# Optimization experiments

Hardware: AMD Instinct MI355X
Metric: run time of the kernel (lower is better)

Reference implementation:

```python
import jax, jax.numpy as jnp
import numpy as np

D_IN, D_OUT, K = 128, 256, 16
B, N = 2, 16384
D_HALF = D_OUT // 2
EPS = 1e-6
GROUPS = 16


def conv1x1(x, w, b):
    # x: (B,C,N,K), w: (O,C), b: (O,)
    return jnp.einsum('oc,bcnk->bonk', w, x) + b[None, :, None, None]


def groupnorm(x, w, b, groups=GROUPS):
    Bv, C, Nv, Kv = x.shape
    xr = x.reshape(Bv, groups, C // groups, Nv, Kv)
    m = xr.mean(axis=(2, 3, 4), keepdims=True)
    v = xr.var(axis=(2, 3, 4), keepdims=True)
    xn = ((xr - m) / jnp.sqrt(v + EPS)).reshape(Bv, C, Nv, Kv)
    return xn * w[None, :, None, None] + b[None, :, None, None]


def lse(coords, x, idx, dist, w, b, gw, gb):
    # coords: (B,N,3); x: (B,C,N,1); idx: (B,N,K); dist: (B,N,K)
    nbr = jax.vmap(lambda c, i: c[i])(coords, idx)          # (B,N,K,3)
    ctr = jnp.broadcast_to(coords[:, :, None, :], nbr.shape)  # (B,N,K,3)
    rel = jnp.concatenate([ctr, nbr, ctr - nbr], axis=-1)    # (B,N,K,9)
    geo = jnp.concatenate([rel.transpose(0, 3, 1, 2), dist[:, None, :, :]], axis=1)  # (B,10,N,K)
    geo = jax.nn.relu(groupnorm(conv1x1(geo, w, b), gw, gb))  # (B,d/2,N,K)
    nf = jax.vmap(lambda f, i: f[:, i])(x[..., 0], idx)       # (B,d/2,N,K)
    return jnp.concatenate([geo, nf], axis=1)                 # (B,d,N,K)


def attentive_pool(x, w, b, gw, gb):
    m = x.mean(axis=-1, keepdims=True)  # (B,C,N,1)
    return jax.nn.relu(groupnorm(conv1x1(m, w, b), gw, gb))


def setup_inputs() -> dict:
    key = jax.random.key(0)
    ks = jax.random.split(key, 16)
    s = 0.02
    d = {
        'coords': jax.random.normal(ks[0], (B, N, 3), jnp.float32),
        'features': jax.random.normal(ks[1], (B, D_IN, N, 1), jnp.float32),
        'knn_dist': jax.random.uniform(ks[2], (B, N, K), jnp.float32),
        'knn_idx': jax.random.randint(ks[3], (B, N, K), 0, N),
        'w1': jax.random.normal(ks[4], (D_HALF, D_IN), jnp.float32) * s,
        'b1': jnp.zeros((D_HALF,), jnp.float32),
        'lse1_w': jax.random.normal(ks[5], (D_HALF, 10), jnp.float32) * s,
        'lse1_b': jnp.zeros((D_HALF,), jnp.float32),
        'lse1_gw': jnp.ones((D_HALF,), jnp.float32),
        'lse1_gb': jnp.zeros((D_HALF,), jnp.float32),
        'pool1_w': jax.random.normal(ks[6], (D_HALF, D_OUT), jnp.float32) * s,
        'pool1_b': jnp.zeros((D_HALF,), jnp.float32),
        'pool1_gw': jnp.ones((D_HALF,), jnp.float32),
        'pool1_gb': jnp.zeros((D_HALF,), jnp.float32),
        'lse2_w': jax.random.normal(ks[7], (D_HALF, 10), jnp.float32) * s,
        'lse2_b': jnp.zeros((D_HALF,), jnp.float32),
        'lse2_gw': jnp.ones((D_HALF,), jnp.float32),
        'lse2_gb': jnp.zeros((D_HALF,), jnp.float32),
        'pool2_w': jax.random.normal(ks[8], (D_OUT, D_OUT), jnp.float32) * s,
        'pool2_b': jnp.zeros((D_OUT,), jnp.float32),
        'pool2_gw': jnp.ones((D_OUT,), jnp.float32),
        'pool2_gb': jnp.zeros((D_OUT,), jnp.float32),
        'mlp2_w': jax.random.normal(ks[9], (2 * D_OUT, D_OUT), jnp.float32) * s,
        'mlp2_b': jnp.zeros((2 * D_OUT,), jnp.float32),
        'sc_w': jax.random.normal(ks[10], (2 * D_OUT, D_IN), jnp.float32) * s,
        'sc_b': jnp.zeros((2 * D_OUT,), jnp.float32),
        'sc_gw': jnp.ones((2 * D_OUT,), jnp.float32),
        'sc_gb': jnp.zeros((2 * D_OUT,), jnp.float32),
    }
    return d


def reference(coords, features, knn_dist, knn_idx,
              w1, b1,
              lse1_w, lse1_b, lse1_gw, lse1_gb,
              pool1_w, pool1_b, pool1_gw, pool1_gb,
              lse2_w, lse2_b, lse2_gw, lse2_gb,
              pool2_w, pool2_b, pool2_gw, pool2_gb,
              mlp2_w, mlp2_b, sc_w, sc_b, sc_gw, sc_gb):
    # mlp1: conv + LeakyReLU(0.2), no norm
    x = jax.nn.leaky_relu(conv1x1(features, w1, b1), 0.2)        # (B,d/2,N,1)
    x = lse(coords, x, knn_idx, knn_dist, lse1_w, lse1_b, lse1_gw, lse1_gb)  # (B,d,N,K)
    x = attentive_pool(x, pool1_w, pool1_b, pool1_gw, pool1_gb)  # (B,d/2,N,1)
    x = lse(coords, x, knn_idx, knn_dist, lse2_w, lse2_b, lse2_gw, lse2_gb)  # (B,d,N,K)
    x = attentive_pool(x, pool2_w, pool2_b, pool2_gw, pool2_gb)  # (B,d,N,1)
    main = conv1x1(x, mlp2_w, mlp2_b)                            # (B,2d,N,1)
    short = groupnorm(conv1x1(features, sc_w, sc_b), sc_gw, sc_gb)
    return jax.nn.leaky_relu(main + short, 0.01)                 # (B,2d,N,1)
```

## Files before the change

### kernel.cpp

```cpp
#include <hip/hip_runtime.h>


constexpr int Bc = 2;
constexpr int Nc = 16384;
constexpr int Kc = 16;
constexpr float EPSc = 1e-6f;

typedef __attribute__((ext_vector_type(8))) short short8;
typedef __attribute__((ext_vector_type(4))) short short4v;
typedef __attribute__((ext_vector_type(4))) float floatx4;

__device__ inline short f2bf(float x) {
    union { float f; unsigned u; } v; v.f = x;
    unsigned r = v.u + 0x7fffu + ((v.u >> 16) & 1u);
    return (short)(r >> 16);
}
__device__ inline float bf2f(short s) {
    union { unsigned u; float f; } v;
    v.u = ((unsigned)(unsigned short)s) << 16;
    return v.f;
}

constexpr size_t OW_P1W = 0;
constexpr size_t OW_P2W = OW_P1W + 128*256;
constexpr size_t OW_M2W = OW_P2W + 256*256;
constexpr size_t OW_SCW = OW_M2W + 512*256;
constexpr size_t OW_W1  = OW_SCW + 512*128;
constexpr size_t OW_L1W = OW_W1  + 128*128;
constexpr size_t OW_L2W = OW_L1W + 128*32;
constexpr size_t OW_FB  = OW_L2W + 128*32;
constexpr size_t OW_X1  = OW_FB  + (size_t)Bc*Nc*128;
constexpr size_t OW_M   = OW_X1  + (size_t)Bc*Nc*128;
constexpr size_t OW_Z1  = OW_M   + (size_t)Bc*Nc*256;
constexpr size_t OW_Z2  = OW_Z1  + (size_t)Bc*Nc*128;
constexpr size_t OW_S   = OW_Z2  + (size_t)Bc*Nc*256;

constexpr int CV0 = 128*256;
constexpr int CV1 = CV0 + 256*256;
constexpr int CV2 = CV1 + 512*256;
constexpr int CV3 = CV2 + 512*128;
constexpr int CV4 = CV3 + 128*128;
constexpr int CV5 = CV4 + 128*32;
constexpr int CV6 = CV5 + 128*32;
constexpr int CVTOT = CV6 + 512;
constexpr int PREP_BLKS = (CVTOT + 255) / 256;
constexpr int FEAT_BLKS = Bc * Nc / 64;

__launch_bounds__(256)
__global__ void prep_feat_kernel(const float* __restrict__ p1w,
                                 const float* __restrict__ p2w,
                                 const float* __restrict__ m2w,
                                 const float* __restrict__ scw,
                                 const float* __restrict__ w1,
                                 const float* __restrict__ l1w,
                                 const float* __restrict__ l2w,
                                 short* __restrict__ W16,
                                 float* __restrict__ ST,
                                 const float* __restrict__ fin,
                                 short* __restrict__ fout)
{
    const int blk = blockIdx.x;
    const int tid = threadIdx.x;
    if (blk < PREP_BLKS) {
        int i = blk * 256 + tid;
        if (i < CV0) { W16[OW_P1W + i] = f2bf(p1w[i]); return; }
        if (i < CV1) { int k = i - CV0; W16[OW_P2W + k] = f2bf(p2w[k]); return; }
        if (i < CV2) { int k = i - CV1; W16[OW_M2W + k] = f2bf(m2w[k]); return; }
        if (i < CV3) { int k = i - CV2; W16[OW_SCW + k] = f2bf(scw[k]); return; }
        if (i < CV4) { int k = i - CV3; W16[OW_W1  + k] = f2bf(w1[k]); return; }
        if (i < CV5) { int k = i - CV4; int o = k >> 5, c = k & 31;
                       W16[OW_L1W + k] = (c < 10) ? f2bf(l1w[o*10+c]) : (short)0; return; }
        if (i < CV6) { int k = i - CV5; int o = k >> 5, c = k & 31;
                       W16[OW_L2W + k] = (c < 10) ? f2bf(l2w[o*10+c]) : (short)0; return; }
        { int k = i - CV6; if (k < 512) ST[k] = 0.f; }
        return;
    }
    const int fb  = blk - PREP_BLKS;
    int lane = tid & 63, wave = tid >> 6;
    int bb = fb / (Nc / 64);
    int n  = (fb % (Nc / 64)) * 64 + lane;
    #pragma unroll
    for (int cc = 0; cc < 4; cc++) {
        int c0 = (wave + cc * 4) * 8;
        short8 sv;
        #pragma unroll
        for (int i = 0; i < 8; i++)
            sv[i] = f2bf(fin[((size_t)bb * 128 + c0 + i) * Nc + n]);
        *(short8*)&fout[((size_t)(bb * Nc + n)) * 128 + c0] = sv;
    }
}

__launch_bounds__(256)
__global__ void geo_reduce_kernel(const float* __restrict__ coords,
                                  const int* __restrict__ knn_idx,
                                  const float* __restrict__ knn_dist,
                                  float* __restrict__ dst)
{
    __shared__ float part[4][65];
    const int tid  = threadIdx.x;
    const int b    = blockIdx.y;
    const int base = blockIdx.x * 256 + tid;
    const float* cb  = coords   + (size_t)b * Nc * 3;
    const int*   ib  = knn_idx  + (size_t)b * Nc * Kc;
    const float* db  = knn_dist + (size_t)b * Nc * Kc;

    float acc[65];
    #pragma unroll
    for (int i = 0; i < 65; i++) acc[i] = 0.f;

    #pragma unroll
    for (int it = 0; it < 4; it++) {
        int r = base + it * 65536;
        int n = r >> 4;
        float cx = cb[n*3+0], cy = cb[n*3+1], cz = cb[n*3+2];
        int   j  = ib[r];
        float nx = cb[j*3+0], ny = cb[j*3+1], nz = cb[j*3+2];
        float d  = db[r];
        float g[10] = {cx,cy,cz,nx,ny,nz,cx-nx,cy-ny,cz-nz,d};
        #pragma unroll
        for (int c = 0; c < 10; c++) acc[c] += g[c];
        int idx = 10;
        #pragma unroll
        for (int c = 0; c < 10; c++)
            #pragma unroll
            for (int c2 = c; c2 < 10; c2++) acc[idx++] += g[c] * g[c2];
    }
    #pragma unroll
    for (int i = 0; i < 65; i++) {
        float v = acc[i];
        #pragma unroll
        for (int off = 1; off < 64; off <<= 1) v += __shfl_xor(v, off);
        acc[i] = v;
    }
    int lane = tid & 63, wave = tid >> 6;
    if (lane == 0) {
        #pragma unroll
        for (int i = 0; i < 65; i++) part[wave][i] = acc[i];
    }
    __syncthreads();
    if (tid < 65) {
        float s = part[0][tid] + part[1][tid] + part[2][tid] + part[3][tid];
        atomicAdd(&dst[b * 65 + tid], s);
    }
}

__launch_bounds__(512)
__global__ void lse_param_kernel(const float* __restrict__ geoS,
                                 const float* __restrict__ l1w,
                                 const float* __restrict__ l1b,
                                 const float* __restrict__ l1gw,
                                 const float* __restrict__ l1gb,
                                 const float* __restrict__ l2w,
                                 const float* __restrict__ l2b,
                                 const float* __restrict__ l2gw,
                                 const float* __restrict__ l2gb,
                                 float* __restrict__ lp)
{
    __shared__ float osum[512], osq[512];
    const int tid = threadIdx.x;
    const int s = tid >> 8, r = tid & 255, b = r >> 7, o = r & 127;
    const float* wf = s ? l2w : l1w;
    const float* bf = s ? l2b : l1b;
    const float* gwf = s ? l2gw : l1gw;
    const float* gbf = s ? l2gb : l1gb;
    const float NK = (float)(Nc * Kc);
    const float* S = geoS + b * 65;

    float w[10];
    #pragma unroll
    for (int c = 0; c < 10; c++) w[c] = wf[o * 10 + c];
    float wS = 0.f;
    #pragma unroll
    for (int c = 0; c < 10; c++) wS += w[c] * S[c];
    float q = 0.f;
    {
        int idx = 10;
        #pragma unroll
        for (int c = 0; c < 10; c++)
            #pragma unroll
            for (int c2 = c; c2 < 10; c2++) {
                float t = w[c] * w[c2] * S[idx++];
                q += (c == c2) ? t : 2.f * t;
            }
    }
    float bo = bf[o];
    osum[tid] = NK * bo + wS;
    osq[tid]  = NK * bo * bo + 2.f * bo * wS + q;
    __syncthreads();
    int gb0 = tid & ~7;
    float gs = 0.f, gq = 0.f;
    #pragma unroll
    for (int i = 0; i < 8; i++) { gs += osum[gb0 + i]; gq += osq[gb0 + i]; }
    float cnt  = 8.f * NK;
    float mean = gs / cnt;
    float var  = gq / cnt - mean * mean;
    float iv   = rsqrtf(var + EPSc);
    float psc  = iv * gwf[o];
    float psh  = (bo - mean) * psc + gbf[o];
    lp[s * 512 + b * 256 + o]       = psc;
    lp[s * 512 + b * 256 + 128 + o] = psh;
}

template<int CIN, int COUT, int GROUP_CH, int MODE>
__launch_bounds__(256)
__global__ void gemm_conv(const short* __restrict__ wA,
                          const short* __restrict__ xB,
                          const float* __restrict__ bias,
                          short* __restrict__ outb,
                          float* __restrict__ outf,
                          float* __restrict__ stats,
                          const short* __restrict__ sbuf,
                          const float* __restrict__ st_sc,
                          const float* __restrict__ gw,
                          const float* __restrict__ gb,
                          float sc_cnt,
                          const float* __restrict__ bst,
                          const float* __restrict__ bgw,
                          const float* __restrict__ bgb,
                          float bcnt,
                          const float* __restrict__ bias2,
                          short* __restrict__ outb2)
{
    __shared__ short Abuf[128 * 68];
    __shared__ short Bbuf[128 * 68];
    __shared__ float sstat[32];
    __shared__ float smean[4], sinv[4];
    __shared__ float bsc[256], bsh[256];

    const int tid  = threadIdx.x;
    const int n0   = blockIdx.x * 128;
    const int mo   = blockIdx.y * 128;
    const int b    = blockIdx.z;
    const int lane = tid & 63;
    const int wave = tid >> 6;
    const int wm   = (wave >> 1) * 64;
    const int wn   = (wave & 1) * 64;
    const int l15  = lane & 15;
    const int quad = lane >> 4;
    const bool sc_tile = (MODE == 4) && (mo < 512);

    if constexpr (MODE == 2 || MODE == 4) { if (tid < 32) sstat[tid] = 0.f; }
    if constexpr (MODE == 3) {
        if (tid < 4) {
            int g = (mo >> 5) + tid;
            float s0 = st_sc[(b * 16 + g) * 2 + 0];
            float s1 = st_sc[(b * 16 + g) * 2 + 1];
            float mean = s0 / sc_cnt;
            float var  = s1 / sc_cnt - mean * mean;
            smean[tid] = mean;
            sinv[tid]  = rsqrtf(var + EPSc);
        }
        if (tid < CIN) {
            int g = tid >> 4;
            float s0 = bst[(b * 16 + g) * 2 + 0];
            float s1 = bst[(b * 16 + g) * 2 + 1];
            float mean = s0 / bcnt;
            float var  = s1 / bcnt - mean * mean;
            float inv  = rsqrtf(var + EPSc);
            float sc_  = inv * bgw[tid];
            bsc[tid] = sc_;
            bsh[tid] = bgb[tid] - mean * sc_;
        }
    }

    floatx4 acc[4][4];
    #pragma unroll
    for (int mi = 0; mi < 4; mi++)
        #pragma unroll
        for (int ni = 0; ni < 4; ni++)
            acc[mi][ni] = (floatx4){0.f, 0.f, 0.f, 0.f};

    const short* wAr = wA + (size_t)mo * CIN;
    const short* xBr = xB + (size_t)b * Nc * CIN + (size_t)n0 * CIN;

    for (int c0 = 0; c0 < CIN; c0 += 64) {
        __syncthreads();
        #pragma unroll
        for (int s = 0; s < 4; s++) {
            int e = tid + s * 256;
            int r = e >> 3, q = e & 7;
            *(short8*)&Abuf[r * 68 + q * 8] =
                *(const short8*)(wAr + (size_t)r * CIN + c0 + q * 8);
            short8 v = *(const short8*)(xBr + (size_t)r * CIN + c0 + q * 8);
            if constexpr (MODE == 3) {
                #pragma unroll
                for (int i = 0; i < 8; i++) {
                    int ch = c0 + q * 8 + i;
                    float t = bf2f(v[i]) * bsc[ch] + bsh[ch];
                    v[i] = f2bf(t > 0.f ? t : 0.f);
                }
            }
            *(short8*)&Bbuf[r * 68 + q * 8] = v;
        }
        __syncthreads();

        #pragma unroll
        for (int kk = 0; kk < 2; kk++) {
            short8 af[4], bfr[4];
            #pragma unroll
            for (int mi = 0; mi < 4; mi++)
                af[mi] = *(short8*)&Abuf[(wm + mi * 16 + l15) * 68 + kk * 32 + quad * 8];
            #pragma unroll
            for (int ni = 0; ni < 4; ni++)
                bfr[ni] = *(short8*)&Bbuf[(wn + ni * 16 + l15) * 68 + kk * 32 + quad * 8];
            #pragma unroll
            for (int mi = 0; mi < 4; mi++)
                #pragma unroll
                for (int ni = 0; ni < 4; ni++)
                    acc[mi][ni] = __builtin_amdgcn_mfma_f32_16x16x32_bf16(
                        af[mi], bfr[ni], acc[mi][ni], 0, 0, 0);
        }
    }

    #pragma unroll
    for (int mi = 0; mi < 4; mi++) {
        int rowl = wm + mi * 16 + quad * 4;
        float b4[4], gw4[4], gb4[4];
        #pragma unroll
        for (int r = 0; r < 4; r++) {
            if constexpr (MODE == 4) {
                b4[r] = sc_tile ? bias[mo + rowl + r] : bias2[mo - 512 + rowl + r];
            } else {
                b4[r] = bias[mo + rowl + r];
            }
            if constexpr (MODE == 3) {
                gw4[r] = gw[mo + rowl + r];
                gb4[r] = gb[mo + rowl + r];
            }
        }
        float gs = 0.f, gq = 0.f;
        #pragma unroll
        for (int ni = 0; ni < 4; ni++) {
            int col = n0 + wn + ni * 16 + l15;
            if constexpr (MODE == 3) {
                short4v s4 = *(const short4v*)&sbuf[((size_t)(b * Nc + col)) * 512 + mo + rowl];
                int gl = rowl >> 5;
                #pragma unroll
                for (int r = 0; r < 4; r++) {
                    float v = acc[mi][ni][r] + b4[r];
                    float s = bf2f(s4[r]);
                    float sn = (s - smean[gl]) * sinv[gl] * gw4[r] + gb4[r];
                    float o = v + sn;
                    o = o > 0.f ? o : 0.01f * o;
                    outf[((size_t)b * COUT + mo + rowl + r) * Nc + col] = o;
                }
            } else if constexpr (MODE == 4) {
                short4v sv;
                #pragma unroll
                for (int r = 0; r < 4; r++) {
                    float v = acc[mi][ni][r] + b4[r];
                    if (sc_tile) { gs += v; gq += v * v; }
                    else v = v > 0.f ? v : 0.2f * v;
                    sv[r] = f2bf(v);
                }
                if (sc_tile)
                    *(short4v*)&outb[((size_t)(b * Nc + col)) * 512 + mo + rowl] = sv;
                else
                    *(short4v*)&outb2[((size_t)(b * Nc + col)) * 128 + mo - 512 + rowl] = sv;
            } else {
                short4v sv;
                #pragma unroll
                for (int r = 0; r < 4; r++) {
                    float v = acc[mi][ni][r] + b4[r];
                    if constexpr (MODE == 1) v = v > 0.f ? v : 0.2f * v;
                    if constexpr (MODE == 2) { gs += v; gq += v * v; }
                    sv[r] = f2bf(v);
                }
                *(short4v*)&outb[((size_t)(b * Nc + col)) * COUT + mo + rowl] = sv;
            }
        }
        if ((MODE == 2) || (MODE == 4 && sc_tile)) {
            #pragma unroll
            for (int off = 1; off < 16; off <<= 1) {
                gs += __shfl_xor(gs, off);
                gq += __shfl_xor(gq, off);
            }
            if (l15 == 0) {
                int gl = rowl / GROUP_CH;
                atomicAdd(&sstat[gl * 2 + 0], gs);
                atomicAdd(&sstat[gl * 2 + 1], gq);
            }
        }
    }
    if ((MODE == 2) || (MODE == 4 && sc_tile)) {
        __syncthreads();
        constexpr int NG = 128 / GROUP_CH;
        if (tid < 2 * NG) {
            int g0 = mo / GROUP_CH;
            atomicAdd(&stats[b * 32 + (g0 + (tid >> 1)) * 2 + (tid & 1)], sstat[tid]);
        }
    }
}

template<int PCOUT, int PGROUP>
__launch_bounds__(512)
__global__ void lse_pool_kernel(const float* __restrict__ coords,
                                const int* __restrict__ knn_idx,
                                const float* __restrict__ knn_dist,
                                const short* __restrict__ xprev,
                                const short* __restrict__ wpad,
                                const float* __restrict__ lp,
                                const float* __restrict__ xst,
                                const float* __restrict__ xgw,
                                const float* __restrict__ xgb,
                                float xcnt,
                                const short* __restrict__ pw,
                                const float* __restrict__ pb,
                                float* __restrict__ stats,
                                short* __restrict__ z)
{
    __shared__ short Bbuf[256 * 40];
    __shared__ short mld[64 * 256];
    __shared__ int   jl[1024];
    __shared__ float xscs[128], xshs[128];
    __shared__ float sstat[32];

    const int tid = threadIdx.x;
    const int b   = blockIdx.x >> 8;
    const int n0  = (blockIdx.x & 255) * 64;
    const bool norm = (xst != nullptr);
    const int lane = tid & 63, wave = tid >> 6;
    const int l15 = lane & 15, quad = lane >> 4;

    if (tid < 32) sstat[tid] = 0.f;
    if (norm && tid < 128) {
        int g = tid >> 3;
        float s0 = xst[(b * 16 + g) * 2 + 0];
        float s1 = xst[(b * 16 + g) * 2 + 1];
        float mean = s0 / xcnt;
        float var  = s1 / xcnt - mean * mean;
        float inv  = rsqrtf(var + EPSc);
        float sc_  = inv * xgw[tid];
        xscs[tid] = sc_;
        xshs[tid] = xgb[tid] - mean * sc_;
    }

    short8 af = *(const short8*)(wpad + (wave * 16 + l15) * 32 + quad * 8);
    floatx4 psc = *(const floatx4*)&lp[b * 256 + wave * 16 + quad * 4];
    floatx4 psh = *(const floatx4*)&lp[b * 256 + 128 + wave * 16 + quad * 4];

    const float* cb = coords + (size_t)b * Nc * 3;

    #pragma unroll
    for (int pass = 0; pass < 4; pass++) {
        if (tid < 256) {
            int ptl = tid & 15, k = tid >> 4;
            int p = pass * 16 + ptl;
            int n = n0 + p;
            float cx = cb[n*3+0], cy = cb[n*3+1], cz = cb[n*3+2];
            int   j  = knn_idx[((size_t)b * Nc + n) * Kc + k];
            float nx = cb[j*3+0], ny = cb[j*3+1], nz = cb[j*3+2];
            float d  = knn_dist[((size_t)b * Nc + n) * Kc + k];
            int col = k * 16 + ptl;
            short8 w0, w1, zz;
            w0[0]=f2bf(cx); w0[1]=f2bf(cy); w0[2]=f2bf(cz);
            w0[3]=f2bf(nx); w0[4]=f2bf(ny); w0[5]=f2bf(nz);
            w0[6]=f2bf(cx-nx); w0[7]=f2bf(cy-ny);
            w1[0]=f2bf(cz-nz); w1[1]=f2bf(d);
            #pragma unroll
            for (int i = 2; i < 8; i++) w1[i] = 0;
            #pragma unroll
            for (int i = 0; i < 8; i++) zz[i] = 0;
            *(short8*)&Bbuf[col * 40 + 0]  = w0;
            *(short8*)&Bbuf[col * 40 + 8]  = w1;
            *(short8*)&Bbuf[col * 40 + 16] = zz;
            *(short8*)&Bbuf[col * 40 + 24] = zz;
            jl[k * 64 + p] = j;
        }
        __syncthreads();
        {
            float s4[4] = {0.f, 0.f, 0.f, 0.f};
            #pragma unroll
            for (int nb = 0; nb < 8; nb++) {
                short8 f0 = *(short8*)&Bbuf[((nb*2+0)*16 + l15) * 40 + quad * 8];
                short8 f1 = *(short8*)&Bbuf[((nb*2+1)*16 + l15) * 40 + quad * 8];
                floatx4 a0 = __builtin_amdgcn_mfma_f32_16x16x32_bf16(
                    af, f0, (floatx4){0.f, 0.f, 0.f, 0.f}, 0, 0, 0);
                floatx4 a1 = __builtin_amdgcn_mfma_f32_16x16x32_bf16(
                    af, f1, (floatx4){0.f, 0.f, 0.f, 0.f}, 0, 0, 0);
                #pragma unroll
                for (int r = 0; r < 4; r++) {
                    float v0 = a0[r] * psc[r] + psh[r];
                    float v1 = a1[r] * psc[r] + psh[r];
                    s4[r] += (v0 > 0.f ? v0 : 0.f) + (v1 > 0.f ? v1 : 0.f);
                }
            }
            int p = pass * 16 + l15;
            int g = wave * 2 + (quad >> 1);
            short4v sv;
            #pragma unroll
            for (int r = 0; r < 4; r++) sv[r] = f2bf(s4[r] * (1.f / 16.f));
            *(short4v*)&mld[p * 256 + ((g ^ (p & 7)) << 3) + (quad & 1) * 4] = sv;
        }
        __syncthreads();
    }

    {
        const int tp = tid >> 4, cs = tid & 15;
        float sc8[8], sh8[8];
        if (norm) {
            #pragma unroll
            for (int i = 0; i < 8; i++) { sc8[i] = xscs[cs*8+i]; sh8[i] = xshs[cs*8+i]; }
        }
        #pragma unroll
        for (int pp = 0; pp < 2; pp++) {
            int p = tp + pp * 32;
            float acc8[8];
            #pragma unroll
            for (int i = 0; i < 8; i++) acc8[i] = 0.f;
            #pragma unroll
            for (int k = 0; k < 16; k++) {
                int j = jl[k * 64 + p];
                short8 v = *(const short8*)&xprev[((size_t)(b * Nc + j)) * 128 + cs * 8];
                if (norm) {
                    #pragma unroll
                    for (int i = 0; i < 8; i++) {
                        float t = bf2f(v[i]) * sc8[i] + sh8[i];
                        acc8[i] += t > 0.f ? t : 0.f;
                    }
                } else {
                    #pragma unroll
                    for (int i = 0; i < 8; i++) acc8[i] += bf2f(v[i]);
                }
            }
            short8 sv;
            #pragma unroll
            for (int i = 0; i < 8; i++) sv[i] = f2bf(acc8[i] * (1.f / 16.f));
            int g = 16 + cs;
            *(short8*)&mld[p * 256 + ((g ^ (p & 7)) << 3)] = sv;
        }
    }
    __syncthreads();

    constexpr int NOT = PCOUT / 128;
    #pragma unroll
    for (int oi = 0; oi < NOT; oi++) {
        const int ot = wave + oi * 8;
        short8 afk[8];
        #pragma unroll
        for (int ks = 0; ks < 8; ks++)
            afk[ks] = *(const short8*)(pw + ((size_t)(ot * 16 + l15)) * 256 + ks * 32 + quad * 8);
        floatx4 acc[4];
        #pragma unroll
        for (int nt = 0; nt < 4; nt++) acc[nt] = (floatx4){0.f, 0.f, 0.f, 0.f};
        #pragma unroll
        for (int ks = 0; ks < 8; ks++) {
            #pragma unroll
            for (int nt = 0; nt < 4; nt++) {
                int p = nt * 16 + l15;
                int g = ks * 4 + quad;
                short8 bfr = *(short8*)&mld[p * 256 + ((g ^ (p & 7)) << 3)];
                acc[nt] = __builtin_amdgcn_mfma_f32_16x16x32_bf16(
                    afk[ks], bfr, acc[nt], 0, 0, 0);
            }
        }
        floatx4 b4 = *(const floatx4*)&pb[ot * 16 + quad * 4];
        float gs = 0.f, gq = 0.f;
        #pragma unroll
        for (int nt = 0; nt < 4; nt++) {
            int col = n0 + nt * 16 + l15;
            short4v sv;
            #pragma unroll
            for (int r = 0; r < 4; r++) {
                float v = acc[nt][r] + b4[r];
                gs += v; gq += v * v;
                sv[r] = f2bf(v);
            }
            *(short4v*)&z[((size_t)(b * Nc + col)) * PCOUT + ot * 16 + quad * 4] = sv;
        }
        #pragma unroll
        for (int off = 1; off < 16; off <<= 1) {
            gs += __shfl_xor(gs, off);
            gq += __shfl_xor(gq, off);
        }
        if (l15 == 0) {
            int gl = (ot * 16 + quad * 4) / PGROUP;
            atomicAdd(&sstat[gl * 2 + 0], gs);
            atomicAdd(&sstat[gl * 2 + 1], gq);
        }
    }
    __syncthreads();
    if (tid < 32) atomicAdd(&stats[b * 32 + tid], sstat[tid]);
}

extern "C" void kernel_launch(void* const* d_in, const int* in_sizes, int n_in,
                              void* d_out, int out_size, void* d_ws, size_t ws_size,
                              hipStream_t stream)
{
    const float* coords   = (const float*)d_in[0];
    const float* features = (const float*)d_in[1];
    const float* knn_dist = (const float*)d_in[2];
    const int*   knn_idx  = (const int*)  d_in[3];
    const float* w1       = (const float*)d_in[4];
    const float* b1       = (const float*)d_in[5];
    const float* lse1_w   = (const float*)d_in[6];
    const float* lse1_b   = (const float*)d_in[7];
    const float* lse1_gw  = (const float*)d_in[8];
    const float* lse1_gb  = (const float*)d_in[9];
    const float* pool1_w  = (const float*)d_in[10];
    const float* pool1_b  = (const float*)d_in[11];
    const float* pool1_gw = (const float*)d_in[12];
    const float* pool1_gb = (const float*)d_in[13];
    const float* lse2_w   = (const float*)d_in[14];
    const float* lse2_b   = (const float*)d_in[15];
    const float* lse2_gw  = (const float*)d_in[16];
    const float* lse2_gb  = (const float*)d_in[17];
    const float* pool2_w  = (const float*)d_in[18];
    const float* pool2_b  = (const float*)d_in[19];
    const float* pool2_gw = (const float*)d_in[20];
    const float* pool2_gb = (const float*)d_in[21];
    const float* mlp2_w   = (const float*)d_in[22];
    const float* mlp2_b   = (const float*)d_in[23];
    const float* sc_w     = (const float*)d_in[24];
    const float* sc_b     = (const float*)d_in[25];
    const float* sc_gw    = (const float*)d_in[26];
    const float* sc_gb    = (const float*)d_in[27];
    (void)in_sizes; (void)n_in; (void)out_size; (void)ws_size;

    float* ST = (float*)d_ws;
    float* ST_SC  = ST + 0;
    float* ST_P1  = ST + 64;
    float* ST_P2  = ST + 128;
    float* ST_GEO = ST + 256;
    float* ST_LP  = ST + 512;
    short* W16 = (short*)(ST + 2048);
    short* P1Wb = W16 + OW_P1W;
    short* P2Wb = W16 + OW_P2W;
    short* M2Wb = W16 + OW_M2W;
    short* SCWb = W16 + OW_SCW;
    short* L1Wb = W16 + OW_L1W;
    short* L2Wb = W16 + OW_L2W;
    short* FB   = W16 + OW_FB;
    short* X1B  = W16 + OW_X1;
    short* Z1   = W16 + OW_Z1;
    short* Z2   = W16 + OW_Z2;
    short* SB   = W16 + OW_S;
    float* out  = (float*)d_out;

    prep_feat_kernel<<<PREP_BLKS + FEAT_BLKS, 256, 0, stream>>>(
        pool1_w, pool2_w, mlp2_w, sc_w, w1, lse1_w, lse2_w, W16, ST,
        features, FB);
    geo_reduce_kernel<<<dim3(256, Bc), 256, 0, stream>>>(
        coords, knn_idx, knn_dist, ST_GEO);
    lse_param_kernel<<<1, 512, 0, stream>>>(
        ST_GEO, lse1_w, lse1_b, lse1_gw, lse1_gb,
        lse2_w, lse2_b, lse2_gw, lse2_gb, ST_LP);

    gemm_conv<128,640,32,4><<<dim3(Nc/128, 5, Bc), 256, 0, stream>>>(
        SCWb, FB, sc_b, SB, nullptr, ST_SC, nullptr, nullptr, nullptr, nullptr, 0.f,
        nullptr, nullptr, nullptr, 0.f, b1, X1B);
    lse_pool_kernel<128,8><<<Bc * Nc / 64, 512, 0, stream>>>(
        coords, knn_idx, knn_dist, X1B, L1Wb, ST_LP,
        nullptr, nullptr, nullptr, 0.f,
        P1Wb, pool1_b, ST_P1, Z1);
    lse_pool_kernel<256,16><<<Bc * Nc / 64, 512, 0, stream>>>(
        coords, knn_idx, knn_dist, Z1, L2Wb, ST_LP + 512,
        ST_P1, pool1_gw, pool1_gb, (float)(8 * Nc),
        P2Wb, pool2_b, ST_P2, Z2);
    gemm_conv<256,512,32,3><<<dim3(Nc/128, 4, Bc), 256, 0, stream>>>(
        M2Wb, Z2, mlp2_b, nullptr, out, nullptr, SB, ST_SC, sc_gw, sc_gb,
        (float)(32 * Nc), ST_P2, pool2_gw, pool2_gb, (float)(16 * Nc),
        nullptr, nullptr);
}
```

Measured before the change: 286.5 us.

## Fuse geo reduction into prep kernel and stage shortcut tile through LDS

Merges the geometry second-moment reduction into the weight/feature prep launch, cutting one kernel launch. The per-block partial sums are now written to a scratch buffer instead of accumulated with atomics, and the single-block parameter kernel sums them. The final GEMM epilogue now loads the shortcut bf16 tile into shared memory with coalesced 16-byte loads, replacing scattered 8-byte global reads. This adds extra syncs and a serial 256-step reduction in the parameter kernel, and reuses the workspace region at OW_M as scratch.

```diff
diff --git a/kernel.cpp b/kernel.cpp
--- a/kernel.cpp
+++ b/kernel.cpp
@@ -45,27 +45,33 @@
 constexpr int CVTOT = CV6 + 512;
 constexpr int PREP_BLKS = (CVTOT + 255) / 256;
 constexpr int FEAT_BLKS = Bc * Nc / 64;
+constexpr int GEO_BLKS  = 256 * Bc;
 
 __launch_bounds__(256)
-__global__ void prep_feat_kernel(const float* __restrict__ p1w,
-                                 const float* __restrict__ p2w,
-                                 const float* __restrict__ m2w,
-                                 const float* __restrict__ scw,
-                                 const float* __restrict__ w1,
-                                 const float* __restrict__ l1w,
-                                 const float* __restrict__ l2w,
-                                 short* __restrict__ W16,
-                                 float* __restrict__ ST,
-                                 const float* __restrict__ fin,
-                                 short* __restrict__ fout)
+__global__ void prep_feat_geo_kernel(const float* __restrict__ p1w,
+                                     const float* __restrict__ p2w,
+                                     const float* __restrict__ m2w,
+                                     const float* __restrict__ scw,
+                                     const float* __restrict__ w1,
+                                     const float* __restrict__ l1w,
+                                     const float* __restrict__ l2w,
+                                     short* __restrict__ W16,
+                                     float* __restrict__ ST,
+                                     const float* __restrict__ fin,
+                                     short* __restrict__ fout,
+                                     const float* __restrict__ coords,
+                                     const int* __restrict__ knn_idx,
+                                     const float* __restrict__ knn_dist,
+                                     float* __restrict__ gp)
 {
+    __shared__ float part[4][65];
     const int blk = blockIdx.x;
     const int tid = threadIdx.x;
     if (blk < PREP_BLKS) {
         int i = blk * 256 + tid;
         if (i < CV0) { W16[OW_P1W + i] = f2bf(p1w[i]); return; }
         if (i < CV1) { int k = i - CV0; W16[OW_P2W + k] = f2bf(p2w[k]); return; }
-        if (i < CV2) { int k = i - CV1; W16[OW_M2W + k] = f2bf(m2w[k]); return; }
+        if (i < CV1 + 512*256) { int k = i - CV1; W16[OW_M2W + k] = f2bf(m2w[k]); return; }
         if (i < CV3) { int k = i - CV2; W16[OW_SCW + k] = f2bf(scw[k]); return; }
         if (i < CV4) { int k = i - CV3; W16[OW_W1  + k] = f2bf(w1[k]); return; }
         if (i < CV5) { int k = i - CV4; int o = k >> 5, c = k & 31;
@@ -75,31 +81,26 @@
         { int k = i - CV6; if (k < 512) ST[k] = 0.f; }
         return;
     }
-    const int fb  = blk - PREP_BLKS;
-    int lane = tid & 63, wave = tid >> 6;
-    int bb = fb / (Nc / 64);
-    int n  = (fb % (Nc / 64)) * 64 + lane;
-    #pragma unroll
-    for (int cc = 0; cc < 4; cc++) {
-        int c0 = (wave + cc * 4) * 8;
-        short8 sv;
-        #pragma unroll
-        for (int i = 0; i < 8; i++)
-            sv[i] = f2bf(fin[((size_t)bb * 128 + c0 + i) * Nc + n]);
-        *(short8*)&fout[((size_t)(bb * Nc + n)) * 128 + c0] = sv;
-    }
-}
-
-__launch_bounds__(256)
-__global__ void geo_reduce_kernel(const float* __restrict__ coords,
-                                  const int* __restrict__ knn_idx,
-                                  const float* __restrict__ knn_dist,
-                                  float* __restrict__ dst)
-{
-    __shared__ float part[4][65];
-    const int tid  = threadIdx.x;
-    const int b    = blockIdx.y;
-    const int base = blockIdx.x * 256 + tid;
+    if (blk < PREP_BLKS + FEAT_BLKS) {
+        const int fb  = blk - PREP_BLKS;
+        int lane = tid & 63, wave = tid >> 6;
+        int bb = fb / (Nc / 64);
+        int n  = (fb % (Nc / 64)) * 64 + lane;
+        #pragma unroll
+        for (int cc = 0; cc < 4; cc++) {
+            int c0 = (wave + cc * 4) * 8;
+            short8 sv;
+            #pragma unroll
+            for (int i = 0; i < 8; i++)
+                sv[i] = f2bf(fin[((size_t)bb * 128 + c0 + i) * Nc + n]);
+            *(short8*)&fout[((size_t)(bb * Nc + n)) * 128 + c0] = sv;
+        }
+        return;
+    }
+    const int g2   = blk - PREP_BLKS - FEAT_BLKS;
+    const int gx   = g2 & 255;
+    const int b    = g2 >> 8;
+    const int base = gx * 256 + tid;
     const float* cb  = coords   + (size_t)b * Nc * 3;
     const int*   ib  = knn_idx  + (size_t)b * Nc * Kc;
     const float* db  = knn_dist + (size_t)b * Nc * Kc;
@@ -139,13 +140,13 @@
     }
     __syncthreads();
     if (tid < 65) {
-        float s = part[0][tid] + part[1][tid] + part[2][tid] + part[3][tid];
-        atomicAdd(&dst[b * 65 + tid], s);
+        gp[((size_t)(b * 256 + gx)) * 65 + tid] =
+            part[0][tid] + part[1][tid] + part[2][tid] + part[3][tid];
     }
 }
 
 __launch_bounds__(512)
-__global__ void lse_param_kernel(const float* __restrict__ geoS,
+__global__ void lse_param_kernel(const float* __restrict__ gp,
                                  const float* __restrict__ l1w,
                                  const float* __restrict__ l1b,
                                  const float* __restrict__ l1gw,
@@ -156,15 +157,26 @@
                                  const float* __restrict__ l2gb,
                                  float* __restrict__ lp)
 {
+    __shared__ float S2[2][65];
     __shared__ float osum[512], osq[512];
     const int tid = threadIdx.x;
+    if (tid < 130) {
+        int bb = tid / 65, i = tid % 65;
+        float s = 0.f;
+        #pragma unroll 8
+        for (int p = 0; p < 256; p++)
+            s += gp[((size_t)(bb * 256 + p)) * 65 + i];
+        S2[bb][i] = s;
+    }
+    __syncthreads();
+
     const int s = tid >> 8, r = tid & 255, b = r >> 7, o = r & 127;
     const float* wf = s ? l2w : l1w;
     const float* bf = s ? l2b : l1b;
     const float* gwf = s ? l2gw : l1gw;
     const float* gbf = s ? l2gb : l1gb;
     const float NK = (float)(Nc * Kc);
-    const float* S = geoS + b * 65;
+    const float* S = S2[b];
 
     float w[10];
     #pragma unroll
@@ -221,11 +233,12 @@
                           const float* __restrict__ bias2,
                           short* __restrict__ outb2)
 {
-    __shared__ short Abuf[128 * 68];
-    __shared__ short Bbuf[128 * 68];
+    __shared__ short SMEM[2 * 128 * 68];
     __shared__ float sstat[32];
     __shared__ float smean[4], sinv[4];
     __shared__ float bsc[256], bsh[256];
+    short* Abuf = SMEM;
+    short* Bbuf = SMEM + 128 * 68;
 
     const int tid  = threadIdx.x;
     const int n0   = blockIdx.x * 128;
@@ -312,6 +325,18 @@
         }
     }
 
+    if constexpr (MODE == 3) {
+        __syncthreads();
+        #pragma unroll
+        for (int s = 0; s < 8; s++) {
+            int e = tid + s * 256;
+            int r = e >> 4, c8 = e & 15;
+            *(short8*)&SMEM[r * 136 + c8 * 8] =
+                *(const short8*)(sbuf + ((size_t)(b * Nc + n0 + r)) * 512 + mo + c8 * 8);
+        }
+        __syncthreads();
+    }
+
     #pragma unroll
     for (int mi = 0; mi < 4; mi++) {
         int rowl = wm + mi * 16 + quad * 4;
@@ -333,7 +358,7 @@
         for (int ni = 0; ni < 4; ni++) {
             int col = n0 + wn + ni * 16 + l15;
             if constexpr (MODE == 3) {
-                short4v s4 = *(const short4v*)&sbuf[((size_t)(b * Nc + col)) * 512 + mo + rowl];
+                short4v s4 = *(const short4v*)&SMEM[(wn + ni * 16 + l15) * 136 + rowl];
                 int gl = rowl >> 5;
                 #pragma unroll
                 for (int r = 0; r < 4; r++) {
@@ -621,7 +646,6 @@
     float* ST_SC  = ST + 0;
     float* ST_P1  = ST + 64;
     float* ST_P2  = ST + 128;
-    float* ST_GEO = ST + 256;
     float* ST_LP  = ST + 512;
     short* W16 = (short*)(ST + 2048);
     short* P1Wb = W16 + OW_P1W;
@@ -632,18 +656,17 @@
     short* L2Wb = W16 + OW_L2W;
     short* FB   = W16 + OW_FB;
     short* X1B  = W16 + OW_X1;
+    float* GEOP = (float*)(W16 + OW_M);
     short* Z1   = W16 + OW_Z1;
     short* Z2   = W16 + OW_Z2;
     short* SB   = W16 + OW_S;
     float* out  = (float*)d_out;
 
-    prep_feat_kernel<<<PREP_BLKS + FEAT_BLKS, 256, 0, stream>>>(
+    prep_feat_geo_kernel<<<PREP_BLKS + FEAT_BLKS + GEO_BLKS, 256, 0, stream>>>(
         pool1_w, pool2_w, mlp2_w, sc_w, w1, lse1_w, lse2_w, W16, ST,
-        features, FB);
-    geo_reduce_kernel<<<dim3(256, Bc), 256, 0, stream>>>(
-        coords, knn_idx, knn_dist, ST_GEO);
+        features, FB, coords, knn_idx, knn_dist, GEOP);
     lse_param_kernel<<<1, 512, 0, stream>>>(
-        ST_GEO, lse1_w, lse1_b, lse1_gw, lse1_gb,
+        GEOP, lse1_w, lse1_b, lse1_gw, lse1_gb,
         lse2_w, lse2_b, lse2_gw, lse2_gb, ST_LP);
 
     gemm_conv<128,640,32,4><<<dim3(Nc/128, 5, Bc), 256, 0, stream>>>(
```

Result: slower. 329.6 us (+15.0%).
